# Kernel optimization log

Measured on AMD Instinct MI355X. Metric: run time of the kernel, lower is better.

The kernel has to match this reference:

```python
import jax, jax.numpy as jnp
import numpy as np

FEAT_STRIDE = 16
PRE_NMS_TOP_N = 6000
POST_NMS_TOP_N = 300
NMS_THRESH = 0.7
MIN_SIZE = 16.0
NEG_INF = -1e30


def _generate_anchors(base_size=16, ratios=(0.5, 1.0, 2.0), scales=(8, 16, 32)):
    """Standard Faster R-CNN anchor generation (ratio-major, scales fastest)."""
    ratios = np.asarray(ratios, np.float32)
    scales = np.asarray(scales, np.float32)
    size = float(base_size * base_size)
    xc = yc = 0.5 * (base_size - 1)
    ws_r = np.round(np.sqrt(size / ratios))          # per-ratio widths
    hs_r = np.round(ws_r * ratios)                   # per-ratio heights
    ws = (ws_r[:, None] * scales[None, :]).ravel()   # [A]
    hs = (hs_r[:, None] * scales[None, :]).ravel()
    anchors = np.stack([xc - 0.5 * (ws - 1), yc - 0.5 * (hs - 1),
                        xc + 0.5 * (ws - 1), yc + 0.5 * (hs - 1)], axis=1)
    return anchors.astype(np.float32)                # [A, 4]


def setup_inputs() -> dict:
    key = jax.random.key(0)
    k1, k2 = jax.random.split(key)
    B, A, H, W = 8, 9, 128, 128
    scores = jax.random.normal(k1, (B, 2 * A, H, W), dtype=jnp.float32)
    bbox_deltas = jax.random.normal(k2, (B, 4 * A, H, W), dtype=jnp.float32) * 0.5
    im_info = jnp.tile(jnp.array([[H * FEAT_STRIDE, W * FEAT_STRIDE, 1.0]],
                                 dtype=jnp.float32), (B, 1))
    anchors = jnp.asarray(_generate_anchors())       # [9, 4]
    return {"scores": scores, "bbox_deltas": bbox_deltas,
            "im_info": im_info, "anchors": anchors}


def _nms_keep(boxes):
    """Greedy NMS keep-mask for boxes sorted by descending score. boxes: [P,4]."""
    P = boxes.shape[0]
    x1, y1, x2, y2 = boxes[:, 0], boxes[:, 1], boxes[:, 2], boxes[:, 3]
    areas = (x2 - x1 + 1.0) * (y2 - y1 + 1.0)
    idx = jnp.arange(P)

    def body(i, keep):
        xx1 = jnp.maximum(x1[i], x1)
        yy1 = jnp.maximum(y1[i], y1)
        xx2 = jnp.minimum(x2[i], x2)
        yy2 = jnp.minimum(y2[i], y2)
        inter = jnp.maximum(0.0, xx2 - xx1 + 1.0) * jnp.maximum(0.0, yy2 - yy1 + 1.0)
        iou = inter / (areas[i] + areas - inter)
        suppress = (iou > NMS_THRESH) & (idx > i) & keep[i]
        return keep & ~suppress

    return jax.lax.fori_loop(0, P, body, jnp.ones((P,), dtype=bool))


def reference(scores, bbox_deltas, im_info, anchors):
    A = anchors.shape[0]
    B, _, H, W = bbox_deltas.shape
    fg_scores = scores[:, A:, :, :]                                   # [B,A,H,W]

    # anchor shifting: [K,4] grid offsets + [A,4] base anchors -> [K*A,4]
    shift_x = jnp.arange(W, dtype=jnp.float32) * FEAT_STRIDE
    shift_y = jnp.arange(H, dtype=jnp.float32) * FEAT_STRIDE
    sx, sy = jnp.meshgrid(shift_x, shift_y)                           # [H,W]
    shifts = jnp.stack([sx.ravel(), sy.ravel(), sx.ravel(), sy.ravel()], axis=1)
    all_anchors = (shifts[:, None, :] + anchors[None, :, :]).reshape(-1, 4)  # [K*A,4]

    # [B,4A,H,W] -> [B,K*A,4], anchor index fastest (matches anchor layout)
    deltas = bbox_deltas.transpose(0, 2, 3, 1).reshape(B, -1, 4)
    scr = fg_scores.transpose(0, 2, 3, 1).reshape(B, -1)              # [B,K*A]

    # bbox_transform_inv
    aw = all_anchors[:, 2] - all_anchors[:, 0] + 1.0
    ah = all_anchors[:, 3] - all_anchors[:, 1] + 1.0
    acx = all_anchors[:, 0] + 0.5 * aw
    acy = all_anchors[:, 1] + 0.5 * ah
    dx, dy, dw, dh = deltas[..., 0], deltas[..., 1], deltas[..., 2], deltas[..., 3]
    pcx = dx * aw + acx
    pcy = dy * ah + acy
    pw = jnp.exp(dw) * aw
    ph = jnp.exp(dh) * ah
    x1 = pcx - 0.5 * pw
    y1 = pcy - 0.5 * ph
    x2 = pcx + 0.5 * pw
    y2 = pcy + 0.5 * ph

    # clip to image
    im_h = im_info[:, 0:1]
    im_w = im_info[:, 1:2]
    x1 = jnp.clip(x1, 0.0, im_w - 1.0)
    y1 = jnp.clip(y1, 0.0, im_h - 1.0)
    x2 = jnp.clip(x2, 0.0, im_w - 1.0)
    y2 = jnp.clip(y2, 0.0, im_h - 1.0)
    boxes = jnp.stack([x1, y1, x2, y2], axis=-1)                      # [B,K*A,4]

    # min-size filtering (mask scores instead of removing boxes)
    min_sz = MIN_SIZE * im_info[:, 2:3]
    valid = ((x2 - x1 + 1.0) >= min_sz) & ((y2 - y1 + 1.0) >= min_sz)
    scr = jnp.where(valid, scr, NEG_INF)

    # pre-NMS top-N by score
    top_scr, top_idx = jax.lax.top_k(scr, PRE_NMS_TOP_N)              # [B,P]
    props = jnp.take_along_axis(boxes, top_idx[..., None], axis=1)    # [B,P,4]

    # greedy NMS per image
    keep = jax.lax.stop_gradient(jax.vmap(_nms_keep)(props))          # [B,P] bool

    # stable-sort kept boxes first (preserves score order), take post-NMS top-N
    order = jnp.argsort((~keep).astype(jnp.int32), axis=1, stable=True)[:, :POST_NMS_TOP_N]
    sel = jnp.take_along_axis(props, order[..., None], axis=1)        # [B,post,4]
    sel_valid = jnp.take_along_axis(keep, order, axis=1)
    sel = sel * sel_valid[..., None].astype(sel.dtype)                # zero-pad invalid

    batch_col = jnp.broadcast_to(
        jnp.arange(sel.shape[0], dtype=sel.dtype)[:, None, None],
        (sel.shape[0], POST_NMS_TOP_N, 1))
    return jnp.concatenate([batch_col, sel], axis=-1)                 # [B,post,5]
```

## Files before the change

kernel.cpp:

```cpp
#include <hip/hip_runtime.h>
#include <stdint.h>

#define FEAT_STRIDE_I 16
#define A_NUM 9
#define HH 128
#define WW 128
#define NPIX (HH * WW)
#define N_ANCH (NPIX * A_NUM)
#define B_NUM 8
#define PRE_NMS 6000
#define POST_NMS 300
#define NMS_THRESH_F 0.7f
#define MIN_SIZE_F 16.0f
#define NEG_INF_F -1e30f

#define NBS 16384
#define SWS(i) ((i) + ((i) >> 5))
#define SWB(bin) ((((bin) & 1023) << 4) | ((bin) >> 10))
#define SEGL 8192
#define QKEYS (N_ANCH / 4)

#define RT_TILES 94
#define GT_TILES 600
#define BQWORDS (RT_TILES * RT_TILES * 64)

#define R_SPLIT 16
#define ROWS_SPLIT (R_SPLIT * 64)
#define G_HEAD 180
#define G_TAIL (GT_TILES - G_HEAD)
#define STATE_STRIDE 2048
#define TMQ (ROWS_SPLIT * RT_TILES)

#define OFF_KEYS    0u
#define OFF_PHIST   4718592u
#define OFF_TMASK   0u
#define OFF_BOXES   6815744u
#define OFF_BBRO    7583744u
#define OFF_BBMUT   8108032u
#define OFF_CNT     8632320u
#define OFF_SEG     8632832u
#define OFF_RIDX    9157120u
#define OFF_STATE   9349120u
#define OFF_MASK    9365504u
#define MASK_BYTES ((size_t)B_NUM * BQWORDS * 8)

__device__ __forceinline__ unsigned sortable_f32(float f) {
    unsigned u = __float_as_uint(f);
    return (u & 0x80000000u) ? ~u : (u | 0x80000000u);
}

__device__ __forceinline__ void decode_box(
    int b, int idx,
    const float* __restrict__ deltas, const float* __restrict__ im_info,
    const float* __restrict__ anchors,
    float& x1, float& y1, float& x2, float& y2, bool& valid)
{
    int a   = idx % A_NUM;
    int pix = idx / A_NUM;
    int w   = pix & (WW - 1);
    int h   = pix >> 7;

    float a0 = anchors[a * 4 + 0];
    float a1 = anchors[a * 4 + 1];
    float a2 = anchors[a * 4 + 2];
    float a3 = anchors[a * 4 + 3];

    float aw = __fadd_rn(__fsub_rn(a2, a0), 1.0f);
    float ah = __fadd_rn(__fsub_rn(a3, a1), 1.0f);
    float sx = (float)(w * FEAT_STRIDE_I);
    float sy = (float)(h * FEAT_STRIDE_I);
    float acx = __fadd_rn(__fadd_rn(sx, a0), __fmul_rn(0.5f, aw));
    float acy = __fadd_rn(__fadd_rn(sy, a1), __fmul_rn(0.5f, ah));

    size_t base = ((size_t)b * 36 + 4 * a) * NPIX + pix;
    float dx = deltas[base];
    float dy = deltas[base + NPIX];
    float dw = deltas[base + 2 * (size_t)NPIX];
    float dh = deltas[base + 3 * (size_t)NPIX];

    float pcx = __fadd_rn(__fmul_rn(dx, aw), acx);
    float pcy = __fadd_rn(__fmul_rn(dy, ah), acy);
    float pw  = __fmul_rn(expf(dw), aw);
    float ph  = __fmul_rn(expf(dh), ah);

    float hx = __fmul_rn(0.5f, pw);
    float hy = __fmul_rn(0.5f, ph);
    x1 = __fsub_rn(pcx, hx);
    y1 = __fsub_rn(pcy, hy);
    x2 = __fadd_rn(pcx, hx);
    y2 = __fadd_rn(pcy, hy);

    float im_h = im_info[b * 3 + 0];
    float im_w = im_info[b * 3 + 1];
    float sc   = im_info[b * 3 + 2];
    float wmax = __fsub_rn(im_w, 1.0f);
    float hmax = __fsub_rn(im_h, 1.0f);

    x1 = fminf(fmaxf(x1, 0.0f), wmax);
    y1 = fminf(fmaxf(y1, 0.0f), hmax);
    x2 = fminf(fmaxf(x2, 0.0f), wmax);
    y2 = fminf(fmaxf(y2, 0.0f), hmax);

    float min_sz = __fmul_rn(MIN_SIZE_F, sc);
    valid = (__fadd_rn(__fsub_rn(x2, x1), 1.0f) >= min_sz) &&
            (__fadd_rn(__fsub_rn(y2, y1), 1.0f) >= min_sz);
}

__global__ void k_decode(
    const float* __restrict__ scores, const float* __restrict__ deltas,
    const float* __restrict__ im_info, const float* __restrict__ anchors,
    unsigned* __restrict__ keys)
{
    int gt = blockIdx.x * blockDim.x + threadIdx.x;
    if (gt >= B_NUM * N_ANCH) return;
    int pix  = gt & (NPIX - 1);
    int rest = gt >> 14;
    int a = rest % A_NUM;
    int b = rest / A_NUM;
    int idx = pix * A_NUM + a;

    float x1, y1, x2, y2; bool valid;
    decode_box(b, idx, deltas, im_info, anchors, x1, y1, x2, y2, valid);

    float s = scores[((size_t)b * 18 + 9 + a) * NPIX + pix];
    if (!valid) s = NEG_INF_F;
    keys[gt] = sortable_f32(s);
}

__global__ __launch_bounds__(1024) void k_hist_part(
    const unsigned* __restrict__ keys, unsigned* __restrict__ phist)
{
    __shared__ unsigned h[SWS(NBS - 1) + 2];
    int b = blockIdx.x >> 2;
    int p = blockIdx.x & 3;
    int t = threadIdx.x;

    for (int i = t; i < SWS(NBS - 1) + 2; i += 1024) h[i] = 0u;
    __syncthreads();

    const uint4* kb4 = (const uint4*)(keys + (size_t)b * N_ANCH + p * QKEYS);
    uint4 v[9];
    #pragma unroll
    for (int k = 0; k < 9; ++k) v[k] = kb4[t + 1024 * k];
    #pragma unroll
    for (int k = 0; k < 9; ++k) {
        atomicAdd(&h[SWS(v[k].x >> 18)], 1u);
        atomicAdd(&h[SWS(v[k].y >> 18)], 1u);
        atomicAdd(&h[SWS(v[k].z >> 18)], 1u);
        atomicAdd(&h[SWS(v[k].w >> 18)], 1u);
    }
    __syncthreads();

    unsigned* ph = phist + (size_t)blockIdx.x * NBS;
    for (int i = t; i < NBS; i += 1024) ph[i] = h[SWS(i)];
}

__global__ __launch_bounds__(1024) void k_thresh2(
    const unsigned* __restrict__ phist, unsigned* __restrict__ bbro,
    unsigned* __restrict__ bbmut, unsigned* __restrict__ thresh,
    unsigned* __restrict__ cnt)
{
    __shared__ unsigned h[SWS(NBS - 1) + 2];
    __shared__ unsigned csum[1024];
    __shared__ unsigned sT;

    int b = blockIdx.x;
    int t = threadIdx.x;
    if (t == 0) sT = 0;

    const unsigned* ph = phist + (size_t)b * 4 * NBS;
    for (int i = t; i < NBS; i += 1024) {
        unsigned s0 = ph[i];
        unsigned s1 = ph[NBS + i];
        unsigned s2 = ph[2 * NBS + i];
        unsigned s3 = ph[3 * NBS + i];
        h[SWS(i)] = s0 + s1 + s2 + s3;
    }
    __syncthreads();

    int base = t * 16;
    unsigned s = 0;
    for (int u = 0; u < 16; ++u) s += h[SWS(base + u)];
    csum[t] = s;
    __syncthreads();
    for (int off = 1; off < 1024; off <<= 1) {
        unsigned v = (t + off < 1024) ? csum[t + off] : 0u;
        __syncthreads();
        csum[t] += v;
        __syncthreads();
    }
    unsigned before = csum[t] - s;

    unsigned acc = before;
    for (int bin = base + 15; bin >= base; --bin) {
        unsigned hh = h[SWS(bin)];
        if (acc + hh >= PRE_NMS) { atomicMax(&sT, (unsigned)bin); break; }
        acc += hh;
    }
    __syncthreads();
    unsigned T = sT;

    acc = before;
    for (int bin = base + 15; bin >= base; --bin) {
        unsigned hh = h[SWS(bin)];
        if ((unsigned)bin == T) cnt[b] = acc + hh;
        h[SWS(bin)] = acc;
        acc += hh;
    }
    if (t == 0) thresh[b] = T;
    __syncthreads();

    unsigned* r = bbro + (size_t)b * NBS;
    unsigned* m = bbmut + (size_t)b * NBS;
    for (int i = t; i < NBS; i += 1024) {
        unsigned v = h[SWS(i)];
        r[i] = v;
        m[SWB(i)] = v;
    }
}

__global__ void k_scatter(
    const unsigned* __restrict__ keys, const unsigned* __restrict__ thresh,
    unsigned* __restrict__ bbmut, unsigned long long* __restrict__ seg)
{
    int gt = blockIdx.x * blockDim.x + threadIdx.x;
    int pix  = gt & (NPIX - 1);
    int rest = gt >> 14;
    int a = rest % A_NUM;
    int b = rest / A_NUM;

    unsigned key = keys[gt];
    unsigned bin = key >> 18;
    if (bin >= thresh[b]) {
        unsigned pos = atomicAdd(&bbmut[(size_t)b * NBS + SWB(bin)], 1u);
        if (pos < SEGL) {
            unsigned idx = (unsigned)(pix * A_NUM + a);
            seg[(size_t)b * SEGL + pos] =
                ((unsigned long long)key << 32) | (unsigned long long)(0xFFFFFFFFu - idx);
        }
    }
}

__global__ __launch_bounds__(256) void k_rank(
    const unsigned long long* __restrict__ seg, const unsigned* __restrict__ cnt,
    const unsigned* __restrict__ bbro, unsigned* __restrict__ ridx)
{
    int b = blockIdx.x >> 5;
    int p = ((blockIdx.x & 31) << 8) + threadIdx.x;
    unsigned n = cnt[b];
    if (n > SEGL) n = SEGL;
    if (p >= (int)n) return;

    const unsigned long long* S = seg + (size_t)b * SEGL;
    unsigned long long key = S[p];
    unsigned bin = (unsigned)(key >> 50);
    const unsigned* bb = bbro + (size_t)b * NBS;
    unsigned base = bb[bin];
    unsigned end = (bin > 0) ? bb[bin - 1] : n;
    if (end > n) end = n;

    unsigned rank = base;
    unsigned q = base;
    for (; q + 8 <= end; q += 8) {
        unsigned long long v0 = S[q + 0], v1 = S[q + 1];
        unsigned long long v2 = S[q + 2], v3 = S[q + 3];
        unsigned long long v4 = S[q + 4], v5 = S[q + 5];
        unsigned long long v6 = S[q + 6], v7 = S[q + 7];
        rank += (unsigned)(v0 > key) + (unsigned)(v1 > key)
              + (unsigned)(v2 > key) + (unsigned)(v3 > key)
              + (unsigned)(v4 > key) + (unsigned)(v5 > key)
              + (unsigned)(v6 > key) + (unsigned)(v7 > key);
    }
    for (; q < end; ++q) rank += (unsigned)(S[q] > key);

    if (rank < PRE_NMS)
        ridx[(size_t)b * PRE_NMS + rank] = 0xFFFFFFFFu - (unsigned)(key & 0xFFFFFFFFull);
}

__global__ void k_decode2(
    const unsigned* __restrict__ ridx,
    const float* __restrict__ deltas, const float* __restrict__ im_info,
    const float* __restrict__ anchors, float* __restrict__ boxes)
{
    int gt = blockIdx.x * blockDim.x + threadIdx.x;
    if (gt >= B_NUM * PRE_NMS) return;
    int b = gt / PRE_NMS;
    int idx = (int)ridx[gt];
    float x1, y1, x2, y2; bool v;
    decode_box(b, idx, deltas, im_info, anchors, x1, y1, x2, y2, v);
    *(float4*)(boxes + (size_t)gt * 4) = make_float4(x1, y1, x2, y2);
}

__device__ __forceinline__ unsigned long long iou_row(
    float4 bi, float ia, float jx1, float jy1, float jx2, float jy2, float ja)
{
    float xx1 = fmaxf(bi.x, jx1);
    float yy1 = fmaxf(bi.y, jy1);
    float xx2 = fminf(bi.z, jx2);
    float yy2 = fminf(bi.w, jy2);
    float iw = fmaxf(0.0f, __fadd_rn(__fsub_rn(xx2, xx1), 1.0f));
    float ih = fmaxf(0.0f, __fadd_rn(__fsub_rn(yy2, yy1), 1.0f));
    float inter = __fmul_rn(iw, ih);
    float uni = __fsub_rn(__fadd_rn(ia, ja), inter);
    float diff = __fsub_rn(inter, __fmul_rn(NMS_THRESH_F, uni));
    unsigned long long sup = __ballot(diff > 0.0f);
    unsigned long long band = __ballot(fabsf(diff) <= __fmul_rn(6e-7f, uni));
    if (band) {
        unsigned long long supd = __ballot(__fdiv_rn(inter, uni) > NMS_THRESH_F);
        sup = (sup & ~band) | (supd & band);
    }
    return sup;
}

__global__ __launch_bounds__(256) void k_iou_mask(
    const float* __restrict__ boxes, unsigned long long* __restrict__ mask,
    int Rstart, int ngroups, const char* __restrict__ statep)
{
    int bid = blockIdx.x;
    int b = bid / ngroups;
    int g = bid - b * ngroups;
    if (statep && ((const int*)(statep + (size_t)b * STATE_STRIDE))[1]) return;

    int R = Rstart;
    while (g >= ((RT_TILES - R + 7) >> 3)) { g -= (RT_TILES - R + 7) >> 3; ++R; }

    int wave = threadIdx.x >> 6;
    int lane = threadIdx.x & 63;
    const float* Bb = boxes + (size_t)b * PRE_NMS * 4;

    __shared__ float4 rb4[64];
    __shared__ float rba[64];
    if (threadIdx.x < 64) {
        int il = R * 64 + threadIdx.x;
        float4 rv = make_float4(0.f, 0.f, -1.f, -1.f);
        if (il < PRE_NMS) rv = *(const float4*)(Bb + 4 * (size_t)il);
        rb4[threadIdx.x] = rv;
        rba[threadIdx.x] = __fmul_rn(__fadd_rn(__fsub_rn(rv.z, rv.x), 1.0f),
                                     __fadd_rn(__fsub_rn(rv.w, rv.y), 1.0f));
    }
    __syncthreads();

    int C1 = R + g * 8 + wave * 2;
    int C2 = C1 + 1;
    if (C1 >= RT_TILES) return;

    float j1x1 = 0.f, j1y1 = 0.f, j1x2 = -1.f, j1y2 = -1.f;
    float j2x1 = 0.f, j2y1 = 0.f, j2x2 = -1.f, j2y2 = -1.f;
    int j1 = C1 * 64 + lane;
    int j2 = C2 * 64 + lane;
    if (j1 < PRE_NMS) {
        float4 v = *(const float4*)(Bb + 4 * (size_t)j1);
        j1x1 = v.x; j1y1 = v.y; j1x2 = v.z; j1y2 = v.w;
    }
    if (C2 < RT_TILES && j2 < PRE_NMS) {
        float4 v = *(const float4*)(Bb + 4 * (size_t)j2);
        j2x1 = v.x; j2y1 = v.y; j2x2 = v.z; j2y2 = v.w;
    }
    float j1a = __fmul_rn(__fadd_rn(__fsub_rn(j1x2, j1x1), 1.0f),
                          __fadd_rn(__fsub_rn(j1y2, j1y1), 1.0f));
    float j2a = __fmul_rn(__fadd_rn(__fsub_rn(j2x2, j2x1), 1.0f),
                          __fadd_rn(__fsub_rn(j2y2, j2y1), 1.0f));

    unsigned long long w1 = 0ULL, w2 = 0ULL;
    if (C1 == R) {
        #pragma unroll 4
        for (int ri = 0; ri < 64; ++ri) {
            float4 bi = rb4[ri];
            float ia = rba[ri];
            unsigned long long s1 = iou_row(bi, ia, j1x1, j1y1, j1x2, j1y2, j1a)
                                    & (0xFFFFFFFFFFFFFFFEull << ri);
            unsigned long long s2 = iou_row(bi, ia, j2x1, j2y1, j2x2, j2y2, j2a);
            w1 = (lane == ri) ? s1 : w1;
            w2 = (lane == ri) ? s2 : w2;
        }
    } else {
        #pragma unroll 4
        for (int ri = 0; ri < 64; ++ri) {
            float4 bi = rb4[ri];
            float ia = rba[ri];
            unsigned long long s1 = iou_row(bi, ia, j1x1, j1y1, j1x2, j1y2, j1a);
            unsigned long long s2 = iou_row(bi, ia, j2x1, j2y1, j2x2, j2y2, j2a);
            w1 = (lane == ri) ? s1 : w1;
            w2 = (lane == ri) ? s2 : w2;
        }
    }

    unsigned long long* Mb = mask + (size_t)b * BQWORDS;
    Mb[(size_t)(R * RT_TILES + C1) * 64 + lane] = w1;
    if (C2 < RT_TILES)
        Mb[(size_t)(R * RT_TILES + C2) * 64 + lane] = w2;
}

__global__ __launch_bounds__(1024) void k_transpose(
    const unsigned long long* __restrict__ mask,
    unsigned long long* __restrict__ tmask)
{
    __shared__ unsigned long long tile[64 * RT_TILES];
    int b = blockIdx.x >> 4;
    int R = blockIdx.x & 15;
    int t = threadIdx.x;
    const unsigned long long* Mb =
        mask + (size_t)b * BQWORDS + (size_t)R * RT_TILES * 64;
    for (int idx = t; idx < RT_TILES * 64; idx += 1024) {
        int C = idx >> 6, r = idx & 63;
        tile[r * RT_TILES + C] = Mb[(size_t)C * 64 + r];
    }
    __syncthreads();
    unsigned long long* Tb =
        tmask + (size_t)b * TMQ + (size_t)R * 64 * RT_TILES;
    for (int idx = t; idx < 64 * RT_TILES; idx += 1024)
        Tb[idx] = tile[idx];
}

__global__ __launch_bounds__(64) void k_nms_scan_part(
    const unsigned long long* __restrict__ mask,
    const unsigned long long* __restrict__ tmask,
    const float* __restrict__ boxes, float* __restrict__ out,
    char* __restrict__ statep, int row_begin, int row_end, int final_phase)
{
    const int b = blockIdx.x;
    const int l = threadIdx.x;
    char* st = statep + (size_t)b * STATE_STRIDE;
    int* s_meta = (int*)st;
    unsigned long long* s_supp = (unsigned long long*)(st + 16);
    int* s_klist = (int*)(st + 768);

    __shared__ int klist[POST_NMS];
    unsigned long long reg0, reg1;
    int kept, done;

    if (row_begin == 0) {
        reg0 = 0ULL; reg1 = 0ULL;
        kept = 0; done = 0;
    } else {
        kept = s_meta[0];
        done = s_meta[1];
        reg0 = s_supp[l];
        reg1 = (l < RT_TILES - 64) ? s_supp[64 + l] : 0ULL;
        for (int k = l; k < POST_NMS; k += 64) klist[k] = s_klist[k];
    }
    __syncthreads();

    const unsigned long long* __restrict__ M = mask + (size_t)b * BQWORDS;
    const unsigned long long* __restrict__ TM = tmask + (size_t)b * TMQ;
    unsigned long long curw = 0; int curwi = -1;

#define LOADROW_T(p0, p1, i) { \
        int _i = ((i) < ROWS_SPLIT) ? (i) : (ROWS_SPLIT - 1); \
        const unsigned long long* _r = TM + (size_t)_i * RT_TILES; \
        p0 = _r[l]; \
        p1 = (l < RT_TILES - 64) ? _r[64 + l] : 0ULL; }

#define LOADROW(p0, p1, i) { \
        int _i = ((i) < PRE_NMS) ? (i) : (PRE_NMS - 1); \
        int _R = _i >> 6; \
        const unsigned long long* _r = M + (size_t)(_R * RT_TILES) * 64 + (_i & 63); \
        p0 = 0ULL; p1 = 0ULL; \
        if (l >= _R) p0 = _r[l * 64]; \
        if (l < RT_TILES - 64 && 64 + l >= _R) p1 = _r[(64 + l) * 64]; }

#define STEP(i, p0, p1) { \
        if (kept < POST_NMS) { \
            int _wi = (i) >> 6; \
            if (_wi != curwi) { \
                curw = (_wi < 64) ? __shfl(reg0, _wi) : __shfl(reg1, _wi - 64); \
                curwi = _wi; \
            } \
            if (!((curw >> ((i) & 63)) & 1ULL)) { \
                if (l == 0) klist[kept] = (i); \
                unsigned long long _d = (_wi < 64) ? __shfl(p0, _wi) \
                                                   : __shfl(p1, _wi - 64); \
                reg0 |= p0; \
                reg1 |= p1; \
                curw |= _d; \
                ++kept; \
            } \
        } }

    if (!done && kept < POST_NMS) {
        unsigned long long p[16][2];
        if (!final_phase) {
            #pragma unroll
            for (int k = 0; k < 16; ++k) { LOADROW_T(p[k][0], p[k][1], row_begin + k) }
            for (int i = row_begin; i < row_end && kept < POST_NMS; i += 16) {
                #pragma unroll
                for (int k = 0; k < 16; ++k) {
                    STEP(i + k, p[k][0], p[k][1])
                    LOADROW_T(p[k][0], p[k][1], i + 16 + k)
                }
            }
        } else {
            #pragma unroll
            for (int k = 0; k < 16; ++k) { LOADROW(p[k][0], p[k][1], row_begin + k) }
            for (int i = row_begin; i < row_end && kept < POST_NMS; i += 16) {
                #pragma unroll
                for (int k = 0; k < 16; ++k) {
                    STEP(i + k, p[k][0], p[k][1])
                    LOADROW(p[k][0], p[k][1], i + 16 + k)
                }
            }
        }
    }
    __syncthreads();

    if (!final_phase) {
        if (l == 0) { s_meta[0] = kept; s_meta[1] = (kept >= POST_NMS) ? 1 : 0; }
        s_supp[l] = reg0;
        if (l < RT_TILES - 64) s_supp[64 + l] = reg1;
        for (int k = l; k < POST_NMS; k += 64) s_klist[k] = klist[k];
    } else {
        for (int k = l; k < POST_NMS; k += 64) {
            size_t o = ((size_t)b * POST_NMS + k) * 5;
            float x1 = 0.f, y1 = 0.f, x2 = 0.f, y2 = 0.f;
            if (k < kept) {
                int idx = klist[k];
                const float4 v = *(const float4*)(boxes + ((size_t)b * PRE_NMS + idx) * 4);
                x1 = v.x; y1 = v.y; x2 = v.z; y2 = v.w;
            }
            out[o + 0] = (float)b;
            out[o + 1] = x1; out[o + 2] = y1; out[o + 3] = x2; out[o + 4] = y2;
        }
    }
#undef LOADROW_T
#undef LOADROW
#undef STEP
}

__global__ __launch_bounds__(1024) void k_nms_out(
    const float* __restrict__ boxes, float* __restrict__ out)
{
    __shared__ float bx1[PRE_NMS], by1[PRE_NMS], bx2[PRE_NMS], by2[PRE_NMS], bar[PRE_NMS];
    __shared__ unsigned rem[(PRE_NMS + 31) / 32];
    __shared__ int kept_idx[POST_NMS];

    int b = blockIdx.x;
    int t = threadIdx.x;

    for (int p = t; p < PRE_NMS; p += 1024) {
        size_t o = ((size_t)b * PRE_NMS + p) * 4;
        float x1 = boxes[o], y1 = boxes[o + 1], x2 = boxes[o + 2], y2 = boxes[o + 3];
        bx1[p] = x1; by1[p] = y1; bx2[p] = x2; by2[p] = y2;
        bar[p] = __fmul_rn(__fadd_rn(__fsub_rn(x2, x1), 1.0f),
                           __fadd_rn(__fsub_rn(y2, y1), 1.0f));
    }
    for (int p = t; p < (PRE_NMS + 31) / 32; p += 1024) rem[p] = 0u;
    __syncthreads();

    int kept = 0;
    for (int i = 0; i < PRE_NMS && kept < POST_NMS; ++i) {
        if (rem[i >> 5] & (1u << (i & 31))) continue;
        if (t == 0) kept_idx[kept] = i;
        float xi1 = bx1[i], yi1 = by1[i], xi2 = bx2[i], yi2 = by2[i], ai = bar[i];
        for (int j = i + 1 + t; j < PRE_NMS; j += 1024) {
            float xx1 = fmaxf(xi1, bx1[j]);
            float yy1 = fmaxf(yi1, by1[j]);
            float xx2 = fminf(xi2, bx2[j]);
            float yy2 = fminf(yi2, by2[j]);
            float iw = fmaxf(0.0f, __fadd_rn(__fsub_rn(xx2, xx1), 1.0f));
            float ih = fmaxf(0.0f, __fadd_rn(__fsub_rn(yy2, yy1), 1.0f));
            float inter = __fmul_rn(iw, ih);
            if (inter > 0.0f) {
                float uni = __fsub_rn(__fadd_rn(ai, bar[j]), inter);
                float iou = __fdiv_rn(inter, uni);
                if (iou > NMS_THRESH_F) atomicOr(&rem[j >> 5], 1u << (j & 31));
            }
        }
        ++kept;
        __syncthreads();
    }

    for (int k = t; k < POST_NMS; k += 1024) {
        size_t o = ((size_t)b * POST_NMS + k) * 5;
        out[o] = (float)b;
        if (k < kept) {
            int ii = kept_idx[k];
            out[o + 1] = bx1[ii]; out[o + 2] = by1[ii];
            out[o + 3] = bx2[ii]; out[o + 4] = by2[ii];
        } else {
            out[o + 1] = 0.0f; out[o + 2] = 0.0f; out[o + 3] = 0.0f; out[o + 4] = 0.0f;
        }
    }
}

extern "C" void kernel_launch(void* const* d_in, const int* in_sizes, int n_in,
                              void* d_out, int out_size, void* d_ws, size_t ws_size,
                              hipStream_t stream)
{
    const float* scores  = (const float*)d_in[0];
    const float* deltas  = (const float*)d_in[1];
    const float* im_info = (const float*)d_in[2];
    const float* anchors = (const float*)d_in[3];
    float* out = (float*)d_out;
    char* ws = (char*)d_ws;

    unsigned* keys             = (unsigned*)(ws + OFF_KEYS);
    unsigned* phist            = (unsigned*)(ws + OFF_PHIST);
    unsigned long long* tmask  = (unsigned long long*)(ws + OFF_TMASK);
    float* boxes               = (float*)(ws + OFF_BOXES);
    unsigned* bbro             = (unsigned*)(ws + OFF_BBRO);
    unsigned* bbmut            = (unsigned*)(ws + OFF_BBMUT);
    unsigned* thresh           = (unsigned*)(ws + OFF_CNT);
    unsigned* cnt              = thresh + 8;
    unsigned long long* seg    = (unsigned long long*)(ws + OFF_SEG);
    unsigned* ridx             = (unsigned*)(ws + OFF_RIDX);
    char* state                = (char*)(ws + OFF_STATE);
    unsigned long long* mask   = (unsigned long long*)(ws + OFF_MASK);

    int total = B_NUM * N_ANCH;
    int blk = 256;
    k_decode<<<(total + blk - 1) / blk, blk, 0, stream>>>(
        scores, deltas, im_info, anchors, keys);
    k_hist_part<<<B_NUM * 4, 1024, 0, stream>>>(keys, phist);
    k_thresh2<<<B_NUM, 1024, 0, stream>>>(phist, bbro, bbmut, thresh, cnt);
    k_scatter<<<(total + blk - 1) / blk, blk, 0, stream>>>(
        keys, thresh, bbmut, seg);
    k_rank<<<B_NUM * 32, 256, 0, stream>>>(seg, cnt, bbro, ridx);
    k_decode2<<<(B_NUM * PRE_NMS + blk - 1) / blk, blk, 0, stream>>>(
        ridx, deltas, im_info, anchors, boxes);

    if (ws_size >= (size_t)OFF_MASK + MASK_BYTES) {
        k_iou_mask<<<B_NUM * G_HEAD, 256, 0, stream>>>(
            boxes, mask, 0, G_HEAD, (const char*)0);
        k_transpose<<<B_NUM * R_SPLIT, 1024, 0, stream>>>(mask, tmask);
        k_nms_scan_part<<<B_NUM, 64, 0, stream>>>(
            mask, tmask, boxes, out, state, 0, ROWS_SPLIT, 0);
        k_iou_mask<<<B_NUM * G_TAIL, 256, 0, stream>>>(
            boxes, mask, R_SPLIT, G_TAIL, (const char*)state);
        k_nms_scan_part<<<B_NUM, 64, 0, stream>>>(
            mask, tmask, boxes, out, state, ROWS_SPLIT, PRE_NMS, 1);
    } else {
        k_nms_out<<<B_NUM, 1024, 0, stream>>>(boxes, out);
    }
}
```

Baseline: 169.3 us.

## Process NMS suppression mask tile-by-tile using find-first-set over alive bits

Replaces the per-row serial scan in the non-final NMS phase with a per-64-row tile loop. Each lane loads its diagonal tile word, and the survivors inside the tile are resolved with ffs and shuffles on an alive bitmask. Suppression rows are then ORed in only for kept rows, as 8-row batches with a mask. The aim is to skip per-row shuffle and branch work for rows already suppressed, at the cost of loading all 64 rows of a tile whenever any row is kept, and of losing the earlier software prefetch pipeline.

```diff
diff --git a/kernel.cpp b/kernel.cpp
--- a/kernel.cpp
+++ b/kernel.cpp
@@ -443,13 +443,6 @@
 
     const unsigned long long* __restrict__ M = mask + (size_t)b * BQWORDS;
     const unsigned long long* __restrict__ TM = tmask + (size_t)b * TMQ;
-    unsigned long long curw = 0; int curwi = -1;
-
-#define LOADROW_T(p0, p1, i) { \
-        int _i = ((i) < ROWS_SPLIT) ? (i) : (ROWS_SPLIT - 1); \
-        const unsigned long long* _r = TM + (size_t)_i * RT_TILES; \
-        p0 = _r[l]; \
-        p1 = (l < RT_TILES - 64) ? _r[64 + l] : 0ULL; }
 
 #define LOADROW(p0, p1, i) { \
         int _i = ((i) < PRE_NMS) ? (i) : (PRE_NMS - 1); \
@@ -478,18 +471,48 @@
         } }
 
     if (!done && kept < POST_NMS) {
-        unsigned long long p[16][2];
         if (!final_phase) {
-            #pragma unroll
-            for (int k = 0; k < 16; ++k) { LOADROW_T(p[k][0], p[k][1], row_begin + k) }
-            for (int i = row_begin; i < row_end && kept < POST_NMS; i += 16) {
-                #pragma unroll
-                for (int k = 0; k < 16; ++k) {
-                    STEP(i + k, p[k][0], p[k][1])
-                    LOADROW_T(p[k][0], p[k][1], i + 16 + k)
+            for (int T = (row_begin >> 6); T < (row_end >> 6) && kept < POST_NMS; ++T) {
+                int base = T << 6;
+                unsigned long long sup_w = __shfl(reg0, T);
+                unsigned long long alive = ~sup_w;
+                unsigned long long d = TM[(size_t)(base + l) * RT_TILES + T];
+                unsigned long long keptm = 0ULL;
+
+                while (alive && kept < POST_NMS) {
+                    int r = __ffsll(alive) - 1;
+                    if (l == 0) klist[kept] = base + r;
+                    ++kept;
+                    keptm |= (1ULL << r);
+                    unsigned long long dr = __shfl(d, r);
+                    alive &= ~dr;
+                    alive &= ~(1ULL << r);
+                }
+
+                if (keptm && kept < POST_NMS) {
+                    #pragma unroll 1
+                    for (int r0 = 0; r0 < 64; r0 += 8) {
+                        unsigned long long w0[8], w1[8];
+                        #pragma unroll
+                        for (int k = 0; k < 8; ++k) {
+                            const unsigned long long* _r =
+                                TM + (size_t)(base + r0 + k) * RT_TILES;
+                            w0[k] = _r[l];
+                            w1[k] = (l < RT_TILES - 64) ? _r[64 + l] : 0ULL;
+                        }
+                        #pragma unroll
+                        for (int k = 0; k < 8; ++k) {
+                            unsigned long long m =
+                                ((keptm >> (r0 + k)) & 1ULL) ? ~0ULL : 0ULL;
+                            reg0 |= w0[k] & m;
+                            reg1 |= w1[k] & m;
+                        }
+                    }
                 }
             }
         } else {
+            unsigned long long curw = 0; int curwi = -1;
+            unsigned long long p[16][2];
             #pragma unroll
             for (int k = 0; k < 16; ++k) { LOADROW(p[k][0], p[k][1], row_begin + k) }
             for (int i = row_begin; i < row_end && kept < POST_NMS; i += 16) {
@@ -521,7 +544,6 @@
             out[o + 1] = x1; out[o + 2] = y1; out[o + 3] = x2; out[o + 4] = y2;
         }
     }
-#undef LOADROW_T
 #undef LOADROW
 #undef STEP
 }
```

Measured after the change: 171.0 us. Within noise of the previous version (+1.0%).
